# Optimization experiments

Hardware: AMD Instinct MI355X
Metric: run time of the kernel (lower is better)

## Reference

```python
import jax, jax.numpy as jnp
import numpy as np

K = 1024   # codebook size
C = 8      # codebook channels
D = K // C # per-channel code dim = 128
BETA = 0.25
B = 8192   # batch of latent vectors, each of size C*D = K


def setup_inputs() -> dict:
    key = jax.random.key(0)
    k1, k2, k3 = jax.random.split(key, 3)
    latents = jax.random.normal(k1, (B, C * D), dtype=jnp.float32)
    # nn.Embedding(K, D) init: uniform(-1/K, 1/K)
    embedding = jax.random.uniform(k2, (K, D), dtype=jnp.float32,
                                   minval=-1.0 / K, maxval=1.0 / K)
    k = jax.random.randint(k3, (C,), 0, 8, dtype=jnp.int32)
    return {"latents": latents, "embedding": embedding, "k": k}


def reference(latents, embedding, k):
    sg = jax.lax.stop_gradient
    flat = latents.reshape(-1, D)                                  # [B*C, D]
    # squared euclidean distance to every code: [B*C, K]
    dist = (jnp.sum(flat ** 2, axis=1, keepdims=True)
            + jnp.sum(embedding ** 2, axis=1)
            - 2.0 * (flat @ embedding.T))
    order = jnp.argsort(dist, axis=1).reshape(-1, C, K)            # [B, C, K]
    # per channel c, pick the k[c]-th nearest code index
    sel = jnp.take_along_axis(order, k[None, :, None], axis=2)[..., 0]  # [B, C]
    # one-hot @ embedding == plain gather of selected rows
    quantized = embedding[sel.reshape(-1)].reshape(latents.shape)  # [B, C*D]
    commitment_loss = jnp.mean((sg(quantized) - latents) ** 2)
    embedding_loss = jnp.mean((quantized - sg(latents)) ** 2)
    vq_loss = BETA * commitment_loss + embedding_loss
    # straight-through estimator
    quantized_st = latents + sg(quantized - latents)
    return quantized_st, vq_loss
```

## Files before the change

kernel.cpp:

```cpp
#include <hip/hip_runtime.h>

#define KDIM   128
#define NELEM  8388608

typedef __attribute__((ext_vector_type(4))) float f32x4;
typedef __attribute__((ext_vector_type(2))) int   int2v;

__device__ inline f32x4 mfma8(long long a, long long b, f32x4 c) {
  return __builtin_amdgcn_mfma_f32_16x16x32_fp8_fp8(a, b, c, 0, 0, 0);
}
__device__ inline void gload16(const void* g, void* l) {
  __builtin_amdgcn_global_load_lds(
      (const __attribute__((address_space(1))) unsigned*)g,
      (__attribute__((address_space(3))) unsigned*)l, 16, 0, 0);
}
__device__ inline long long pk8(float4 v0, float4 v1) {
  int lo = __builtin_amdgcn_cvt_pk_fp8_f32(v0.x, v0.y, 0, false);
  lo     = __builtin_amdgcn_cvt_pk_fp8_f32(v0.z, v0.w, lo, true);
  int hi = __builtin_amdgcn_cvt_pk_fp8_f32(v1.x, v1.y, 0, false);
  hi     = __builtin_amdgcn_cvt_pk_fp8_f32(v1.z, v1.w, hi, true);
  int2v t; t.x = lo; t.y = hi;
  return __builtin_bit_cast(long long, t);
}
__device__ inline float and_or10(float s, int lo5, unsigned mask) {
  float r;
  asm("v_and_or_b32 %0, %1, %2, %3" : "=v"(r) : "v"(s), "s"(mask), "v"(lo5));
  return r;
}
__device__ inline float max3f(float a, float b, float c) {
  float r;
  asm("v_max3_f32 %0, %1, %2, %3" : "=v"(r) : "v"(a), "v"(b), "v"(c));
  return r;
}
__device__ inline float sumsq(float4 a, float4 b) {
  return a.x*a.x + a.y*a.y + a.z*a.z + a.w*a.w + b.x*b.x + b.y*b.y + b.z*b.z + b.w*b.w;
}
__device__ inline void merge8(float (&t)[8], int msk) {
  float o[8];
#pragma unroll
  for (int p = 0; p < 8; ++p) o[p] = __shfl_xor(t[p], msk);
  float m[8];
#pragma unroll
  for (int p = 0; p < 8; ++p) m[p] = fmaxf(t[p], o[7 - p]);
#pragma unroll
  for (int s = 4; s; s >>= 1)
#pragma unroll
    for (int i = 0; i < 8; ++i)
      if (!(i & s)) {
        float x = fmaxf(m[i], m[i | s]);
        m[i | s] = fminf(m[i], m[i | s]);
        m[i] = x;
      }
#pragma unroll
  for (int p = 0; p < 8; ++p) t[p] = m[p];
}
__device__ inline void ins8(float (&top)[8], float x) {
#pragma unroll
  for (int p = 0; p < 8; ++p) {
    float mx = fmaxf(top[p], x);
    x = fminf(top[p], x);
    top[p] = mx;
  }
}

__global__ void vq_prep(const float* __restrict__ emb, unsigned char* __restrict__ ebf8,
                        float* __restrict__ esqm, unsigned long long* __restrict__ lossAcc,
                        unsigned* __restrict__ cnt) {
  int j = blockIdx.x, d = threadIdx.x;
  float v = emb[j * KDIM + d];
  float vs = v * 1024.0f;
  int p = __builtin_amdgcn_cvt_pk_fp8_f32(vs, vs, 0, false);
  ebf8[j * KDIM + (d ^ ((j & 15) << 3))] = (unsigned char)(p & 0xFF);
  float s = v * v;
#pragma unroll
  for (int m = 1; m <= 32; m <<= 1) s += __shfl_xor(s, m);
  __shared__ float w[2];
  if ((d & 63) == 0) w[d >> 6] = s;
  __syncthreads();
  if (d == 0) esqm[j] = -512.0f * (w[0] + w[1]);
  if (j == 0 && d == 0) { lossAcc[0] = 0ULL; cnt[0] = 0u; }
}

__device__ inline void write_rows(const float* __restrict__ emb, float* __restrict__ outp,
                                  int grow0, int idx, int lane) {
#pragma unroll 4
  for (int r = 0; r < 16; ++r) {
    int s2 = __shfl(idx, r);
    float2 qv = *(const float2*)(emb + (size_t)s2 * KDIM + lane * 2);
    *(float2*)(outp + (size_t)(grow0 + r) * KDIM + lane * 2) = qv;
  }
}

__device__ inline void scan_set(const unsigned char* bk0, const unsigned char* bk1,
                                const unsigned char* bk2, const unsigned char* bk3,
                                const float* esqmLds, int hi, const long long (&b)[4],
                                const int (&c8)[8], float (&top)[8]) {
  const unsigned MASK = 0xFFFFFC00u;
#pragma unroll 4
  for (int g2 = 0; g2 < 16; ++g2) {
    float xp[2];
#pragma unroll
    for (int h = 0; h < 2; ++h) {
      const int g = g2 * 2 + h;
      const int off = g * 4096;
      const float* eb = esqmLds + g * 32 + hi * 4;
      f32x4 e0 = *(const f32x4*)(eb);
      f32x4 e1 = *(const f32x4*)(eb + 16);
      long long t0 = *(const long long*)(bk0 + off);
      long long t1 = *(const long long*)(bk1 + off);
      long long t2 = *(const long long*)(bk2 + off);
      long long t3 = *(const long long*)(bk3 + off);
      long long u0 = *(const long long*)(bk0 + off + 2048);
      long long u1 = *(const long long*)(bk1 + off + 2048);
      long long u2 = *(const long long*)(bk2 + off + 2048);
      long long u3 = *(const long long*)(bk3 + off + 2048);
      f32x4 a0 = mfma8(t0, b[0], e0);
      f32x4 a1 = mfma8(u0, b[0], e1);
      a0 = mfma8(t1, b[1], a0); a1 = mfma8(u1, b[1], a1);
      a0 = mfma8(t2, b[2], a0); a1 = mfma8(u2, b[2], a1);
      a0 = mfma8(t3, b[3], a0); a1 = mfma8(u3, b[3], a1);
      float k0 = and_or10(a0[0], c8[0], MASK), k1 = and_or10(a0[1], c8[1], MASK);
      float k2 = and_or10(a0[2], c8[2], MASK), k3 = and_or10(a0[3], c8[3], MASK);
      float k4 = and_or10(a1[0], c8[4], MASK), k5 = and_or10(a1[1], c8[5], MASK);
      float k6 = and_or10(a1[2], c8[6], MASK), k7 = and_or10(a1[3], c8[7], MASK);
      float m0 = max3f(k0, k1, k2);
      float m1 = max3f(k3, k4, k5);
      float m2 = max3f(k6, k7, m0);
      float x = fmaxf(m1, m2);
      xp[h] = __builtin_bit_cast(float,
              __builtin_bit_cast(unsigned, x) | ((unsigned)g << 5));
    }
    ins8(top, fmaxf(xp[0], xp[1]));
  }
}

__global__ __launch_bounds__(512, 1) void vq_main(
    const float* __restrict__ lat, const float* __restrict__ emb,
    const int* __restrict__ ksel, const unsigned char* __restrict__ ebf8,
    const float* __restrict__ esqm, float* __restrict__ out,
    unsigned long long* __restrict__ lossAcc, unsigned* __restrict__ cnt,
    float* __restrict__ loss) {
  __shared__ __align__(16) unsigned char smem[131072 + 4096 + 64];
  float* esqmLds = (float*)(smem + 131072);
  float* wLds    = (float*)(smem + 131072 + 4096);

  const int tid = threadIdx.x, lane = tid & 63, wid = tid >> 6;
  const int n = lane & 15, hi = lane >> 4;
  const int gR0 = blockIdx.x * 256;

  const float* rp0 = lat + (size_t)(gR0 + wid * 32 + n) * KDIM + hi * 8;
  const float* rp1 = rp0 + 16 * KDIM;
  float4 p0[4], p1[4], q0[4], q1[4];
#pragma unroll
  for (int ks = 0; ks < 4; ++ks) {
    p0[ks] = *(const float4*)(rp0 + ks * 32);
    p1[ks] = *(const float4*)(rp0 + ks * 32 + 4);
    q0[ks] = *(const float4*)(rp1 + ks * 32);
    q1[ks] = *(const float4*)(rp1 + ks * 32 + 4);
  }
  {
    const char* src = (const char*)ebf8 + tid * 16;
    char* dst = (char*)smem + tid * 16;
#pragma unroll
    for (int qq = 0; qq < 16; ++qq) gload16(src + qq * 8192, dst + qq * 8192);
    if (tid < 256) gload16((const char*)esqm + tid * 16, (char*)esqmLds + tid * 16);
  }
  float fsq0, fsq1;
  long long b0[4], b1[4];
  {
    float s0 = 0.f, s1 = 0.f;
#pragma unroll
    for (int ks = 0; ks < 4; ++ks) {
      s0 += sumsq(p0[ks], p1[ks]);
      s1 += sumsq(q0[ks], q1[ks]);
    }
    s0 += __shfl_xor(s0, 16); s0 += __shfl_xor(s0, 32);
    s1 += __shfl_xor(s1, 16); s1 += __shfl_xor(s1, 32);
    fsq0 = s0; fsq1 = s1;
#pragma unroll
    for (int ks = 0; ks < 4; ++ks) {
      b0[ks] = pk8(p0[ks], p1[ks]);
      b1[ks] = pk8(q0[ks], q1[ks]);
    }
  }
  asm volatile("s_waitcnt vmcnt(0)" ::: "memory");
  __builtin_amdgcn_s_barrier();

  const unsigned char* ab = smem + n * 128 + ((hi ^ (n & 3)) << 3);
  const int nh = n >> 2;
  const unsigned char* bk0 = ab + ((0 ^ nh) << 5);
  const unsigned char* bk1 = ab + ((1 ^ nh) << 5);
  const unsigned char* bk2 = ab + ((2 ^ nh) << 5);
  const unsigned char* bk3 = ab + ((3 ^ nh) << 5);

  int c8[8];
#pragma unroll
  for (int r = 0; r < 4; ++r) { c8[r] = hi * 4 + r; c8[4 + r] = 16 + hi * 4 + r; }

  int kk = ksel[lane & 7];
  kk = kk < 0 ? 0 : (kk > 7 ? 7 : kk);

  const float NINF = __builtin_bit_cast(float, 0xFF800000u);

  float top0[8];
#pragma unroll
  for (int p = 0; p < 8; ++p) top0[p] = NINF;
  scan_set(bk0, bk1, bk2, bk3, esqmLds, hi, b0, c8, top0);
  merge8(top0, 16); merge8(top0, 32);
  float sel0 = top0[0];
#pragma unroll
  for (int p = 1; p < 8; ++p) sel0 = (kk == p) ? top0[p] : sel0;
  unsigned sb0 = __builtin_bit_cast(unsigned, sel0);
  int idx0 = (int)(sb0 & 1023u);
  float rl0 = fsq0 - __builtin_bit_cast(float, sb0 & 0xFFFFFC00u) * (1.0f / 512.0f);
  write_rows(emb, out, gR0 + wid * 32, idx0, lane);

  float top1[8];
#pragma unroll
  for (int p = 0; p < 8; ++p) top1[p] = NINF;
  scan_set(bk0, bk1, bk2, bk3, esqmLds, hi, b1, c8, top1);
  merge8(top1, 16); merge8(top1, 32);
  float sel1 = top1[0];
#pragma unroll
  for (int p = 1; p < 8; ++p) sel1 = (kk == p) ? top1[p] : sel1;
  unsigned sb1 = __builtin_bit_cast(unsigned, sel1);
  int idx1 = (int)(sb1 & 1023u);
  float rl1 = fsq1 - __builtin_bit_cast(float, sb1 & 0xFFFFFC00u) * (1.0f / 512.0f);
  write_rows(emb, out, gR0 + wid * 32 + 16, idx1, lane);

  float c = (lane < 16) ? (rl0 + rl1) : 0.f;
#pragma unroll
  for (int m = 1; m <= 32; m <<= 1) c += __shfl_xor(c, m);
  if (lane == 0) wLds[wid] = c;
  __syncthreads();
  if (tid == 0) {
    double bs = 0.0;
#pragma unroll
    for (int w = 0; w < 8; ++w) bs += (double)wLds[w];
    long long iv = (long long)(bs * 1048576.0 + 0.5);
    atomicAdd(lossAcc, (unsigned long long)iv);
    __threadfence();
    unsigned done = atomicAdd(cnt, 1u);
    if (done == 255u) {
      unsigned long long tot = atomicAdd(lossAcc, 0ULL);
      loss[0] = (float)((double)(long long)tot * (1.25 / (1048576.0 * 8388608.0)));
    }
  }
}

extern "C" void kernel_launch(void* const* d_in, const int* in_sizes, int n_in,
                              void* d_out, int out_size, void* d_ws, size_t ws_size,
                              hipStream_t stream) {
  const float* lat = (const float*)d_in[0];
  const float* emb = (const float*)d_in[1];
  const int* ksel = (const int*)d_in[2];
  float* out = (float*)d_out;

  unsigned char* ebf8 = (unsigned char*)d_ws;
  float* esqm = (float*)((char*)d_ws + 131072);
  unsigned long long* lossAcc =
      (unsigned long long*)((char*)d_ws + 135168);
  unsigned* cnt = (unsigned*)((char*)d_ws + 135176);

  vq_prep<<<1024, 128, 0, stream>>>(emb, ebf8, esqm, lossAcc, cnt);
  vq_main<<<256, 512, 0, stream>>>(lat, emb, ksel, ebf8, esqm, out, lossAcc, cnt,
                                   out + NELEM);
}
```

Before: 44.35 us.

## Switch distance GEMM to 32x32x16 fp8 MFMA with one 32-row pass per wave

```diff
diff --git a/kernel.cpp b/kernel.cpp
--- a/kernel.cpp
+++ b/kernel.cpp
@@ -3,11 +3,12 @@
 #define KDIM   128
 #define NELEM  8388608
 
-typedef __attribute__((ext_vector_type(4))) float f32x4;
-typedef __attribute__((ext_vector_type(2))) int   int2v;
-
-__device__ inline f32x4 mfma8(long long a, long long b, f32x4 c) {
-  return __builtin_amdgcn_mfma_f32_16x16x32_fp8_fp8(a, b, c, 0, 0, 0);
+typedef __attribute__((ext_vector_type(4)))  float f32x4;
+typedef __attribute__((ext_vector_type(16))) float f32x16;
+typedef __attribute__((ext_vector_type(2)))  int   int2v;
+
+__device__ inline f32x16 mfma32(long long a, long long b, f32x16 c) {
+  return __builtin_amdgcn_mfma_f32_32x32x16_fp8_fp8(a, b, c, 0, 0, 0);
 }
 __device__ inline void gload16(const void* g, void* l) {
   __builtin_amdgcn_global_load_lds(
@@ -81,59 +82,6 @@
   if (j == 0 && d == 0) { lossAcc[0] = 0ULL; cnt[0] = 0u; }
 }
 
-__device__ inline void write_rows(const float* __restrict__ emb, float* __restrict__ outp,
-                                  int grow0, int idx, int lane) {
-#pragma unroll 4
-  for (int r = 0; r < 16; ++r) {
-    int s2 = __shfl(idx, r);
-    float2 qv = *(const float2*)(emb + (size_t)s2 * KDIM + lane * 2);
-    *(float2*)(outp + (size_t)(grow0 + r) * KDIM + lane * 2) = qv;
-  }
-}
-
-__device__ inline void scan_set(const unsigned char* bk0, const unsigned char* bk1,
-                                const unsigned char* bk2, const unsigned char* bk3,
-                                const float* esqmLds, int hi, const long long (&b)[4],
-                                const int (&c8)[8], float (&top)[8]) {
-  const unsigned MASK = 0xFFFFFC00u;
-#pragma unroll 4
-  for (int g2 = 0; g2 < 16; ++g2) {
-    float xp[2];
-#pragma unroll
-    for (int h = 0; h < 2; ++h) {
-      const int g = g2 * 2 + h;
-      const int off = g * 4096;
-      const float* eb = esqmLds + g * 32 + hi * 4;
-      f32x4 e0 = *(const f32x4*)(eb);
-      f32x4 e1 = *(const f32x4*)(eb + 16);
-      long long t0 = *(const long long*)(bk0 + off);
-      long long t1 = *(const long long*)(bk1 + off);
-      long long t2 = *(const long long*)(bk2 + off);
-      long long t3 = *(const long long*)(bk3 + off);
-      long long u0 = *(const long long*)(bk0 + off + 2048);
-      long long u1 = *(const long long*)(bk1 + off + 2048);
-      long long u2 = *(const long long*)(bk2 + off + 2048);
-      long long u3 = *(const long long*)(bk3 + off + 2048);
-      f32x4 a0 = mfma8(t0, b[0], e0);
-      f32x4 a1 = mfma8(u0, b[0], e1);
-      a0 = mfma8(t1, b[1], a0); a1 = mfma8(u1, b[1], a1);
-      a0 = mfma8(t2, b[2], a0); a1 = mfma8(u2, b[2], a1);
-      a0 = mfma8(t3, b[3], a0); a1 = mfma8(u3, b[3], a1);
-      float k0 = and_or10(a0[0], c8[0], MASK), k1 = and_or10(a0[1], c8[1], MASK);
-      float k2 = and_or10(a0[2], c8[2], MASK), k3 = and_or10(a0[3], c8[3], MASK);
-      float k4 = and_or10(a1[0], c8[4], MASK), k5 = and_or10(a1[1], c8[5], MASK);
-      float k6 = and_or10(a1[2], c8[6], MASK), k7 = and_or10(a1[3], c8[7], MASK);
-      float m0 = max3f(k0, k1, k2);
-      float m1 = max3f(k3, k4, k5);
-      float m2 = max3f(k6, k7, m0);
-      float x = fmaxf(m1, m2);
-      xp[h] = __builtin_bit_cast(float,
-              __builtin_bit_cast(unsigned, x) | ((unsigned)g << 5));
-    }
-    ins8(top, fmaxf(xp[0], xp[1]));
-  }
-}
-
 __global__ __launch_bounds__(512, 1) void vq_main(
     const float* __restrict__ lat, const float* __restrict__ emb,
     const int* __restrict__ ksel, const unsigned char* __restrict__ ebf8,
@@ -145,18 +93,16 @@
   float* wLds    = (float*)(smem + 131072 + 4096);
 
   const int tid = threadIdx.x, lane = tid & 63, wid = tid >> 6;
-  const int n = lane & 15, hi = lane >> 4;
+  const int r32 = lane & 31, h = lane >> 5;
   const int gR0 = blockIdx.x * 256;
-
-  const float* rp0 = lat + (size_t)(gR0 + wid * 32 + n) * KDIM + hi * 8;
-  const float* rp1 = rp0 + 16 * KDIM;
-  float4 p0[4], p1[4], q0[4], q1[4];
-#pragma unroll
-  for (int ks = 0; ks < 4; ++ks) {
-    p0[ks] = *(const float4*)(rp0 + ks * 32);
-    p1[ks] = *(const float4*)(rp0 + ks * 32 + 4);
-    q0[ks] = *(const float4*)(rp1 + ks * 32);
-    q1[ks] = *(const float4*)(rp1 + ks * 32 + 4);
+  const int row0 = gR0 + wid * 32;
+
+  const float* rp = lat + (size_t)(row0 + r32) * KDIM + h * 8;
+  float4 v0[8], v1[8];
+#pragma unroll
+  for (int i = 0; i < 8; ++i) {
+    v0[i] = *(const float4*)(rp + i * 16);
+    v1[i] = *(const float4*)(rp + i * 16 + 4);
   }
   {
     const char* src = (const char*)ebf8 + tid * 16;
@@ -165,70 +111,96 @@
     for (int qq = 0; qq < 16; ++qq) gload16(src + qq * 8192, dst + qq * 8192);
     if (tid < 256) gload16((const char*)esqm + tid * 16, (char*)esqmLds + tid * 16);
   }
-  float fsq0, fsq1;
-  long long b0[4], b1[4];
+  float fsq;
+  long long b[8];
   {
-    float s0 = 0.f, s1 = 0.f;
-#pragma unroll
-    for (int ks = 0; ks < 4; ++ks) {
-      s0 += sumsq(p0[ks], p1[ks]);
-      s1 += sumsq(q0[ks], q1[ks]);
-    }
-    s0 += __shfl_xor(s0, 16); s0 += __shfl_xor(s0, 32);
-    s1 += __shfl_xor(s1, 16); s1 += __shfl_xor(s1, 32);
-    fsq0 = s0; fsq1 = s1;
-#pragma unroll
-    for (int ks = 0; ks < 4; ++ks) {
-      b0[ks] = pk8(p0[ks], p1[ks]);
-      b1[ks] = pk8(q0[ks], q1[ks]);
-    }
+    float s = 0.f;
+#pragma unroll
+    for (int i = 0; i < 8; ++i) {
+      s += sumsq(v0[i], v1[i]);
+      b[i] = pk8(v0[i], v1[i]);
+    }
+    s += __shfl_xor(s, 32);
+    fsq = s;
   }
   asm volatile("s_waitcnt vmcnt(0)" ::: "memory");
   __builtin_amdgcn_s_barrier();
 
-  const unsigned char* ab = smem + n * 128 + ((hi ^ (n & 3)) << 3);
-  const int nh = n >> 2;
-  const unsigned char* bk0 = ab + ((0 ^ nh) << 5);
-  const unsigned char* bk1 = ab + ((1 ^ nh) << 5);
-  const unsigned char* bk2 = ab + ((2 ^ nh) << 5);
-  const unsigned char* bk3 = ab + ((3 ^ nh) << 5);
-
-  int c8[8];
-#pragma unroll
-  for (int r = 0; r < 4; ++r) { c8[r] = hi * 4 + r; c8[4 + r] = 16 + hi * 4 + r; }
-
+  const unsigned char* aBase[8];
+#pragma unroll
+  for (int i = 0; i < 8; ++i)
+    aBase[i] = smem + r32 * 128 + ((i * 16 + h * 8) ^ ((r32 & 15) << 3));
+
+  int c16[16];
+#pragma unroll
+  for (int rg = 0; rg < 16; ++rg) c16[rg] = (rg & 3) + 8 * (rg >> 2) + 4 * h;
+  const unsigned MASK = 0xFFFFFC00u;
+
+  const float NINF = __builtin_bit_cast(float, 0xFF800000u);
+  float top[8];
+#pragma unroll
+  for (int p = 0; p < 8; ++p) top[p] = NINF;
+
+#pragma unroll 2
+  for (int g2 = 0; g2 < 16; ++g2) {
+    const int gA = g2 * 2, gB = g2 * 2 + 1;
+    f32x16 accA, accB;
+#pragma unroll
+    for (int q = 0; q < 4; ++q) {
+      f32x4 eA = *(const f32x4*)(esqmLds + gA * 32 + h * 4 + q * 8);
+      f32x4 eB = *(const f32x4*)(esqmLds + gB * 32 + h * 4 + q * 8);
+#pragma unroll
+      for (int e = 0; e < 4; ++e) { accA[q * 4 + e] = eA[e]; accB[q * 4 + e] = eB[e]; }
+    }
+#pragma unroll
+    for (int i = 0; i < 8; ++i) {
+      long long aA = *(const long long*)(aBase[i] + gA * 4096);
+      long long aB = *(const long long*)(aBase[i] + gB * 4096);
+      accA = mfma32(aA, b[i], accA);
+      accB = mfma32(aB, b[i], accB);
+    }
+    float xA, xB;
+    {
+      float k[16];
+#pragma unroll
+      for (int rg = 0; rg < 16; ++rg) k[rg] = and_or10(accA[rg], c16[rg], MASK);
+      float p0 = max3f(k[0], k[1], k[2]),  p1 = max3f(k[3], k[4], k[5]);
+      float p2 = max3f(k[6], k[7], k[8]),  p3 = max3f(k[9], k[10], k[11]);
+      float p4 = max3f(k[12], k[13], k[14]);
+      float x = fmaxf(max3f(p0, p1, k[15]), max3f(p2, p3, p4));
+      xA = __builtin_bit_cast(float, __builtin_bit_cast(unsigned, x) | ((unsigned)gA << 5));
+    }
+    {
+      float k[16];
+#pragma unroll
+      for (int rg = 0; rg < 16; ++rg) k[rg] = and_or10(accB[rg], c16[rg], MASK);
+      float p0 = max3f(k[0], k[1], k[2]),  p1 = max3f(k[3], k[4], k[5]);
+      float p2 = max3f(k[6], k[7], k[8]),  p3 = max3f(k[9], k[10], k[11]);
+      float p4 = max3f(k[12], k[13], k[14]);
+      float x = fmaxf(max3f(p0, p1, k[15]), max3f(p2, p3, p4));
+      xB = __builtin_bit_cast(float, __builtin_bit_cast(unsigned, x) | ((unsigned)gB << 5));
+    }
+    ins8(top, fmaxf(xA, xB));
+  }
+
+  merge8(top, 32);
   int kk = ksel[lane & 7];
   kk = kk < 0 ? 0 : (kk > 7 ? 7 : kk);
-
-  const float NINF = __builtin_bit_cast(float, 0xFF800000u);
-
-  float top0[8];
-#pragma unroll
-  for (int p = 0; p < 8; ++p) top0[p] = NINF;
-  scan_set(bk0, bk1, bk2, bk3, esqmLds, hi, b0, c8, top0);
-  merge8(top0, 16); merge8(top0, 32);
-  float sel0 = top0[0];
-#pragma unroll
-  for (int p = 1; p < 8; ++p) sel0 = (kk == p) ? top0[p] : sel0;
-  unsigned sb0 = __builtin_bit_cast(unsigned, sel0);
-  int idx0 = (int)(sb0 & 1023u);
-  float rl0 = fsq0 - __builtin_bit_cast(float, sb0 & 0xFFFFFC00u) * (1.0f / 512.0f);
-  write_rows(emb, out, gR0 + wid * 32, idx0, lane);
-
-  float top1[8];
-#pragma unroll
-  for (int p = 0; p < 8; ++p) top1[p] = NINF;
-  scan_set(bk0, bk1, bk2, bk3, esqmLds, hi, b1, c8, top1);
-  merge8(top1, 16); merge8(top1, 32);
-  float sel1 = top1[0];
-#pragma unroll
-  for (int p = 1; p < 8; ++p) sel1 = (kk == p) ? top1[p] : sel1;
-  unsigned sb1 = __builtin_bit_cast(unsigned, sel1);
-  int idx1 = (int)(sb1 & 1023u);
-  float rl1 = fsq1 - __builtin_bit_cast(float, sb1 & 0xFFFFFC00u) * (1.0f / 512.0f);
-  write_rows(emb, out, gR0 + wid * 32 + 16, idx1, lane);
-
-  float c = (lane < 16) ? (rl0 + rl1) : 0.f;
+  float sel = top[0];
+#pragma unroll
+  for (int p = 1; p < 8; ++p) sel = (kk == p) ? top[p] : sel;
+  unsigned sb = __builtin_bit_cast(unsigned, sel);
+  int idx = (int)(sb & 1023u);
+  float rl = fsq - __builtin_bit_cast(float, sb & 0xFFFFFC00u) * (1.0f / 512.0f);
+
+#pragma unroll 4
+  for (int r = 0; r < 32; ++r) {
+    int s2 = __shfl(idx, r);
+    float2 qv = *(const float2*)(emb + (size_t)s2 * KDIM + lane * 2);
+    *(float2*)(out + (size_t)(row0 + r) * KDIM + lane * 2) = qv;
+  }
+
+  float c = (lane < 32) ? rl : 0.f;
 #pragma unroll
   for (int m = 1; m <= 32; m <<= 1) c += __shfl_xor(c, m);
   if (lane == 0) wLds[wid] = c;
```

Result: faster. 40.66 us (-8.3%).
